# Kernel tuning notes

Hardware: AMD Instinct MI355X
Metric: run time of the kernel (lower is better)

The kernel has to match this reference:

```python
import jax, jax.numpy as jnp
import numpy as np

D = 768      # hidden_size
H = 12       # num_head
HD = D // H  # head_dim
LN_EPS = 1e-5


def setup_inputs() -> dict:
    key = jax.random.key(0)
    ks = jax.random.split(key, 9)
    N, S = 4, 2048
    s = 0.02
    return {
        "hidden_state": jax.random.normal(ks[0], (N, S, D), dtype=jnp.float32),
        "key_padding_mask": jax.random.randint(ks[1], (N, S), 0, 2, dtype=jnp.int64),
        "Wq": jax.random.normal(ks[2], (D, D), dtype=jnp.float32) * s,
        "Wk": jax.random.normal(ks[3], (D, D), dtype=jnp.float32) * s,
        "Wv": jax.random.normal(ks[4], (D, D), dtype=jnp.float32) * s,
        "Wo": jax.random.normal(ks[5], (D, D), dtype=jnp.float32) * s,
        "W1": jax.random.normal(ks[6], (4 * D, D), dtype=jnp.float32) * s,
        "W2": jax.random.normal(ks[7], (D, 4 * D), dtype=jnp.float32) * s,
        "ln_g": jnp.ones((D,), dtype=jnp.float32),
        "ln_b": jnp.zeros((D,), dtype=jnp.float32),
    }


def _layernorm(x, g, b):
    mu = jnp.mean(x, axis=-1, keepdims=True)
    var = jnp.mean(jnp.square(x - mu), axis=-1, keepdims=True)
    return (x - mu) * jax.lax.rsqrt(var + LN_EPS) * g + b


def reference(hidden_state, key_padding_mask, Wq, Wk, Wv, Wo, W1, W2, ln_g, ln_b):
    x = hidden_state
    N, S, _ = x.shape
    # Note: original module projects K and V from `query` (self-attention).
    def proj(W):
        return (x @ W.T).reshape(N, S, H, HD).transpose(0, 2, 1, 3)  # [N,H,S,HD]
    Q, K, V = proj(Wq), proj(Wk), proj(Wv)
    scores = jnp.einsum("bhqd,bhkd->bhqk", Q, K)  # [N,H,S,S]
    # int mask: 0 marks padding positions -> masked with -inf
    pad = (key_padding_mask == 0)[:, None, None, :]  # [N,1,1,S]
    scores = jnp.where(pad, -jnp.inf, scores)
    attn = jax.nn.softmax(scores / np.sqrt(HD), axis=-1)
    ctx = jnp.einsum("bhqk,bhkd->bhqd", attn, V)
    ctx = ctx.transpose(0, 2, 1, 3).reshape(N, S, D)
    mha = ctx @ Wo.T
    # residual + LayerNorm (same LN params used twice, as in the original)
    n1 = _layernorm(x + mha, ln_g, ln_b)
    # FFN with exact GELU (torch nn.GELU default)
    f = jax.nn.gelu(n1 @ W1.T, approximate=False) @ W2.T
    return _layernorm(n1 + f, ln_g, ln_b)
```

## Files before the change

kernel.cpp:

```cpp
#include <hip/hip_runtime.h>
#include <math.h>

typedef unsigned short u16;
typedef unsigned int u32;
typedef __bf16 bf16x8 __attribute__((ext_vector_type(8)));
typedef float f32x4 __attribute__((ext_vector_type(4)));

#define NB 4
#define SS 2048
#define DD 768
#define HH 12
#define HD 64
#define ROWS (NB*SS)

__device__ __forceinline__ u16 f2bf(float f) {
    union { float f; unsigned u; } v; v.f = f;
    unsigned r = v.u + 0x7fffu + ((v.u >> 16) & 1u);
    return (u16)(r >> 16);
}
__device__ __forceinline__ u32 fas(float f) { union { float f; u32 u; } v; v.f = f; return v.u; }

__device__ __forceinline__ void gl_lds16(const void* g, void* l) {
    __builtin_amdgcn_global_load_lds((__attribute__((address_space(1))) void*)(g),
                                     (__attribute__((address_space(3))) void*)(l),
                                     16, 0, 0);
}

__global__ __launch_bounds__(256) void prep_kernel(
        const float* __restrict__ X, const float* __restrict__ Wq,
        const float* __restrict__ Wk, const float* __restrict__ Wv,
        const float* __restrict__ Wo, const float* __restrict__ W1,
        const float* __restrict__ W2, const int* __restrict__ mask,
        u16* __restrict__ Xb, u16* __restrict__ Wqkvb, u16* __restrict__ Wob,
        u16* __restrict__ W1b, u16* __restrict__ W2b, float* __restrict__ mb) {
    const int blk = blockIdx.x, tid = threadIdx.x;
    const float* src; u16* dst; int idx;
    if (blk < 6144)       { src = X;  dst = Xb;               idx = blk * 1024 + tid * 4; }
    else if (blk < 6720)  { src = Wq; dst = Wqkvb;            idx = (blk - 6144) * 1024 + tid * 4; }
    else if (blk < 7296)  { src = Wk; dst = Wqkvb + DD * DD;  idx = (blk - 6720) * 1024 + tid * 4; }
    else if (blk < 7872)  { src = Wv; dst = Wqkvb + 2*DD*DD;  idx = (blk - 7296) * 1024 + tid * 4; }
    else if (blk < 8448)  { src = Wo; dst = Wob;              idx = (blk - 7872) * 1024 + tid * 4; }
    else if (blk < 10752) { src = W1; dst = W1b;              idx = (blk - 8448) * 1024 + tid * 4; }
    else if (blk < 13056) { src = W2; dst = W2b;              idx = (blk - 10752) * 1024 + tid * 4; }
    else {
        int i = (blk - 13056) * 1024 + tid * 4;
        float4 o;
        o.x = mask[i]     == 0 ? -1e30f : 0.0f;
        o.y = mask[i + 1] == 0 ? -1e30f : 0.0f;
        o.z = mask[i + 2] == 0 ? -1e30f : 0.0f;
        o.w = mask[i + 3] == 0 ? -1e30f : 0.0f;
        *(float4*)&mb[i] = o;
        return;
    }
    float4 v = *(const float4*)&src[idx];
    ushort4 o;
    o.x = f2bf(v.x); o.y = f2bf(v.y); o.z = f2bf(v.z); o.w = f2bf(v.w);
    *(ushort4*)&dst[idx] = o;
}

template <int EPI, int BN>
__global__ __launch_bounds__(256) void gemm_bt(const u16* __restrict__ A,
                                               const u16* __restrict__ B,
                                               int M, int N, int K,
                                               void* __restrict__ out,
                                               const void* __restrict__ aux,
                                               u16* __restrict__ Qb,
                                               u16* __restrict__ Kb,
                                               u16* __restrict__ Vb) {
    __shared__ __align__(16) u16 lA[128 * 64];
    __shared__ __align__(16) u16 lB[BN * 64];
    constexpr int MI = (BN == 128) ? 4 : 2;
    const int tid = threadIdx.x;
    const int lane = tid & 63, wave = tid >> 6;
    const int quad = lane >> 4, lc = lane & 15;
    const int m0 = blockIdx.y * 128, n0 = blockIdx.x * BN;
    const int wrow = (BN == 128) ? (wave >> 1) * 64 : wave * 32;
    const int wcol = (BN == 128) ? (wave & 1) * 64 : 0;
    const int swz = lc & 7;

    f32x4 acc[MI][4] = {};

    for (int kb = 0; kb < K; kb += 64) {
        __syncthreads();
#pragma unroll
        for (int p0 = 0; p0 < 1024; p0 += 256) {
            int p = p0 + tid, row = p >> 3, cl = (p & 7) ^ (row & 7);
            gl_lds16(A + (size_t)(m0 + row) * K + kb + cl * 8, &lA[(size_t)(p0 + wave * 64) * 8]);
        }
#pragma unroll
        for (int p0 = 0; p0 < BN * 8; p0 += 256) {
            int p = p0 + tid, row = p >> 3, cl = (p & 7) ^ (row & 7);
            gl_lds16(B + (size_t)(n0 + row) * K + kb + cl * 8, &lB[(size_t)(p0 + wave * 64) * 8]);
        }
        __syncthreads();
#pragma unroll
        for (int k2 = 0; k2 < 2; ++k2) {
            bf16x8 af[MI], bfr[4];
#pragma unroll
            for (int t = 0; t < MI; ++t)
                af[t] = *(const bf16x8*)&lA[(wrow + t * 16 + lc) * 64 + ((quad + k2 * 4) ^ swz) * 8];
#pragma unroll
            for (int t = 0; t < 4; ++t)
                bfr[t] = *(const bf16x8*)&lB[(wcol + t * 16 + lc) * 64 + ((quad + k2 * 4) ^ swz) * 8];
#pragma unroll
            for (int mi = 0; mi < MI; ++mi)
#pragma unroll
                for (int ni = 0; ni < 4; ++ni)
                    acc[mi][ni] = __builtin_amdgcn_mfma_f32_16x16x32_bf16(af[mi], bfr[ni],
                                                                         acc[mi][ni], 0, 0, 0);
        }
    }

#pragma unroll
    for (int mi = 0; mi < MI; ++mi) {
#pragma unroll
        for (int r = 0; r < 4; ++r) {
            int m = m0 + wrow + mi * 16 + quad * 4 + r;
#pragma unroll
            for (int ni = 0; ni < 4; ++ni) {
                int n = n0 + wcol + ni * 16 + lc;
                float v = acc[mi][ni][r];
                if constexpr (EPI == 0) {
                    int b = m >> 11, s = m & 2047;
                    int which = n / DD, rem = n - which * DD;
                    int h = rem >> 6, d = rem & 63;
                    u16* dst = which == 0 ? Qb : (which == 1 ? Kb : Vb);
                    dst[((((size_t)b * HH + h) * SS + s) << 6) + d] = f2bf(v);
                } else if constexpr (EPI == 1) {
                    float u = v * fmaf(v * v, 0.035677408f, 0.7978845608f);
                    float e = __builtin_amdgcn_exp2f(u * 2.885390082f);
                    float g = v - v * __builtin_amdgcn_rcpf(e + 1.0f);
                    ((u16*)out)[(size_t)m * N + n] = f2bf(g);
                } else if constexpr (EPI == 2) {
                    ((float*)out)[(size_t)m * N + n] =
                        v + ((const float*)aux)[(size_t)m * N + n];
                } else {
                    ((float*)out)[(size_t)m * N + n] =
                        v + (float)(((const __bf16*)aux)[(size_t)m * N + n]);
                }
            }
        }
    }
}

__global__ __launch_bounds__(256) void transpose_v(const u16* __restrict__ V,
                                                   u16* __restrict__ Vt) {
    __shared__ u16 t[32][33];
    int bh = blockIdx.z;
    int s0 = blockIdx.x * 32, d0 = blockIdx.y * 32;
    const u16* vb = V + (size_t)bh * SS * HD;
    u16* vtb = Vt + (size_t)bh * HD * SS;
    int tx = threadIdx.x & 31, ty = threadIdx.x >> 5;
#pragma unroll
    for (int i = 0; i < 32; i += 8) t[ty + i][tx] = vb[(size_t)(s0 + ty + i) * HD + d0 + tx];
    __syncthreads();
#pragma unroll
    for (int i = 0; i < 32; i += 8) vtb[(size_t)(d0 + ty + i) * SS + s0 + tx] = t[tx][ty + i];
}

__global__ __launch_bounds__(256) void attn_kernel(const u16* __restrict__ Q,
                                                   const u16* __restrict__ K,
                                                   const u16* __restrict__ Vt,
                                                   const float* __restrict__ maskbias,
                                                   u16* __restrict__ Ctx) {
    __shared__ __align__(16) u16 lK[2][64 * 64];
    __shared__ __align__(16) u16 lV[2][64 * 64];
    __shared__ __align__(16) u16 lP[4][32 * 72];
    const int tid = threadIdx.x, lane = tid & 63, wave = tid >> 6;
    const int quad = lane >> 4, lc = lane & 15;
    const int bh = blockIdx.x % (NB * HH);
    const int b = bh / HH, h = bh - b * HH;
    const int q0 = (blockIdx.x / (NB * HH)) * 128;
    const u16* Qg = Q + ((size_t)bh * SS + q0 + wave * 32) * HD;
    const u16* Kg = K + (size_t)bh * SS * HD;
    const u16* Vg = Vt + (size_t)bh * HD * SS;
    const float* mbg = maskbias + b * SS;
    const int sw = lc & 7;

    const int srow = tid >> 3, scl = (tid & 7) ^ (srow & 7);
    const int srow2 = (256 + tid) >> 3, scl2 = (tid & 7) ^ (srow2 & 7);

    bf16x8 qf[2][2];
#pragma unroll
    for (int mi = 0; mi < 2; ++mi)
#pragma unroll
        for (int k2 = 0; k2 < 2; ++k2)
            qf[mi][k2] = *(const bf16x8*)(Qg + (size_t)(mi * 16 + lc) * HD + k2 * 32 + quad * 8);

    bf16x8 onesf;
#pragma unroll
    for (int i = 0; i < 8; ++i) onesf[i] = (__bf16)1.0f;

    f32x4 oacc[2][4] = {};
    f32x4 lsum[2] = {};

    {
        gl_lds16(Kg + (size_t)srow * HD + scl * 8,        &lK[0][(size_t)(wave * 64) * 8]);
        gl_lds16(Vg + (size_t)srow * SS + scl * 8,        &lV[0][(size_t)(wave * 64) * 8]);
        gl_lds16(Kg + (size_t)srow2 * HD + scl2 * 8,      &lK[0][(size_t)(256 + wave * 64) * 8]);
        gl_lds16(Vg + (size_t)srow2 * SS + scl2 * 8,      &lV[0][(size_t)(256 + wave * 64) * 8]);
    }

    for (int j0 = 0; j0 < SS; j0 += 64) {
        const int cur = (j0 >> 6) & 1;
        __syncthreads();
        if (j0 + 64 < SS) {
            const int nxt = cur ^ 1;
            gl_lds16(Kg + (size_t)(j0 + 64 + srow) * HD + scl * 8,   &lK[nxt][(size_t)(wave * 64) * 8]);
            gl_lds16(Vg + (size_t)srow * SS + j0 + 64 + scl * 8,     &lV[nxt][(size_t)(wave * 64) * 8]);
            gl_lds16(Kg + (size_t)(j0 + 64 + srow2) * HD + scl2 * 8, &lK[nxt][(size_t)(256 + wave * 64) * 8]);
            gl_lds16(Vg + (size_t)srow2 * SS + j0 + 64 + scl2 * 8,   &lV[nxt][(size_t)(256 + wave * 64) * 8]);
        }

        f32x4 sacc[4][2] = {};
#pragma unroll
        for (int k2 = 0; k2 < 2; ++k2)
#pragma unroll
            for (int ni = 0; ni < 4; ++ni) {
                bf16x8 kf = *(const bf16x8*)&lK[cur][(ni * 16 + lc) * 64 + ((quad + k2 * 4) ^ sw) * 8];
                sacc[ni][0] = __builtin_amdgcn_mfma_f32_16x16x32_bf16(kf, qf[0][k2], sacc[ni][0], 0, 0, 0);
                sacc[ni][1] = __builtin_amdgcn_mfma_f32_16x16x32_bf16(kf, qf[1][k2], sacc[ni][1], 0, 0, 0);
            }

#pragma unroll
        for (int ni = 0; ni < 4; ++ni) {
            f32x4 mbv = *(const f32x4*)(mbg + j0 + ni * 16 + quad * 4);
#pragma unroll
            for (int mi = 0; mi < 2; ++mi) {
#pragma unroll
                for (int r = 0; r < 4; ++r)
                    sacc[ni][mi][r] = __builtin_amdgcn_exp2f(fmaf(sacc[ni][mi][r], 0.180336880f, mbv[r]));
                u32 w0 = __builtin_amdgcn_perm(fas(sacc[ni][mi][1]), fas(sacc[ni][mi][0]), 0x07060302);
                u32 w1 = __builtin_amdgcn_perm(fas(sacc[ni][mi][3]), fas(sacc[ni][mi][2]), 0x07060302);
                *(uint2*)&lP[wave][(mi * 16 + lc) * 72 + ni * 16 + quad * 4] = make_uint2(w0, w1);
            }
        }

#pragma unroll
        for (int k2 = 0; k2 < 2; ++k2) {
            bf16x8 pf0 = *(const bf16x8*)&lP[wave][(size_t)lc * 72 + k2 * 32 + quad * 8];
            bf16x8 pf1 = *(const bf16x8*)&lP[wave][(size_t)(16 + lc) * 72 + k2 * 32 + quad * 8];
            lsum[0] = __builtin_amdgcn_mfma_f32_16x16x32_bf16(pf0, onesf, lsum[0], 0, 0, 0);
            lsum[1] = __builtin_amdgcn_mfma_f32_16x16x32_bf16(pf1, onesf, lsum[1], 0, 0, 0);
#pragma unroll
            for (int ni = 0; ni < 4; ++ni) {
                bf16x8 vf = *(const bf16x8*)&lV[cur][(ni * 16 + lc) * 64 + ((quad + k2 * 4) ^ sw) * 8];
                oacc[0][ni] = __builtin_amdgcn_mfma_f32_16x16x32_bf16(pf0, vf, oacc[0][ni], 0, 0, 0);
                oacc[1][ni] = __builtin_amdgcn_mfma_f32_16x16x32_bf16(pf1, vf, oacc[1][ni], 0, 0, 0);
            }
        }
    }

#pragma unroll
    for (int mi = 0; mi < 2; ++mi)
#pragma unroll
        for (int r = 0; r < 4; ++r) {
            float inv = 1.0f / lsum[mi][r];
            int s = q0 + wave * 32 + mi * 16 + quad * 4 + r;
            size_t base = ((size_t)(b * SS + s)) * DD + h * HD;
#pragma unroll
            for (int ni = 0; ni < 4; ++ni)
                Ctx[base + ni * 16 + lc] = f2bf(oacc[mi][ni][r] * inv);
        }
}

__global__ __launch_bounds__(256) void ln_kernel(const float* __restrict__ in,
                                                 const float* __restrict__ g,
                                                 const float* __restrict__ bb,
                                                 u16* __restrict__ out_bf,
                                                 float* __restrict__ out_f) {
    const int row = blockIdx.x, tid = threadIdx.x;
    const float* x = in + (size_t)row * DD;
    float v0 = x[tid], v1 = x[tid + 256], v2 = x[tid + 512];
    float s = v0 + v1 + v2;
    float q = v0 * v0 + v1 * v1 + v2 * v2;
#pragma unroll
    for (int o = 1; o < 64; o <<= 1) {
        s += __shfl_xor(s, o);
        q += __shfl_xor(q, o);
    }
    __shared__ float rs[4], rq[4];
    int wave = tid >> 6;
    if ((tid & 63) == 0) { rs[wave] = s; rq[wave] = q; }
    __syncthreads();
    s = rs[0] + rs[1] + rs[2] + rs[3];
    q = rq[0] + rq[1] + rq[2] + rq[3];
    float mu = s * (1.0f / DD);
    float var = q * (1.0f / DD) - mu * mu;
    float rstd = rsqrtf(var + 1e-5f);
#pragma unroll
    for (int j = 0; j < 3; ++j) {
        int col = tid + j * 256;
        float v = (j == 0 ? v0 : (j == 1 ? v1 : v2));
        float y = (v - mu) * rstd * g[col] + bb[col];
        if (out_bf) out_bf[(size_t)row * DD + col] = f2bf(y);
        if (out_f) out_f[(size_t)row * DD + col] = y;
    }
}

extern "C" void kernel_launch(void* const* d_in, const int* in_sizes, int n_in,
                              void* d_out, int out_size, void* d_ws, size_t ws_size,
                              hipStream_t stream) {
    const float* X    = (const float*)d_in[0];
    const int*   mask = (const int*)d_in[1];
    const float* Wq   = (const float*)d_in[2];
    const float* Wk   = (const float*)d_in[3];
    const float* Wv   = (const float*)d_in[4];
    const float* Wo   = (const float*)d_in[5];
    const float* W1   = (const float*)d_in[6];
    const float* W2   = (const float*)d_in[7];
    const float* ln_g = (const float*)d_in[8];
    const float* ln_b = (const float*)d_in[9];
    float* out = (float*)d_out;

    char* ws = (char*)d_ws;
    size_t off = 0;
    auto alloc = [&](size_t bytes) {
        void* p = ws + off;
        off += (bytes + 255) & ~(size_t)255;
        return p;
    };
    u16*   Xbf   = (u16*)alloc((size_t)ROWS * DD * 2);
    u16*   Wqkvb = (u16*)alloc((size_t)3 * DD * DD * 2);
    u16*   Wob   = (u16*)alloc((size_t)DD * DD * 2);
    u16*   W1b   = (u16*)alloc((size_t)4 * DD * DD * 2);
    u16*   W2b   = (u16*)alloc((size_t)4 * DD * DD * 2);
    float* mbias = (float*)alloc((size_t)NB * SS * 4);
    u16*   Qb    = (u16*)alloc((size_t)ROWS * DD * 2);
    u16*   Kb    = (u16*)alloc((size_t)ROWS * DD * 2);
    u16*   Vb    = (u16*)alloc((size_t)ROWS * DD * 2);
    u16*   Vtb   = (u16*)alloc((size_t)ROWS * DD * 2);
    float* resid = (float*)alloc((size_t)ROWS * DD * 4);
    u16*   n1b   = (u16*)alloc((size_t)ROWS * DD * 2);
    u16*   Gb    = Qb;
    u16*   Ctxb  = Xbf;
    float* h2    = resid;

    prep_kernel<<<dim3(13064), dim3(256), 0, stream>>>(
        X, Wq, Wk, Wv, Wo, W1, W2, mask,
        Xbf, Wqkvb, Wob, W1b, W2b, mbias);

    gemm_bt<0, 128><<<dim3(3 * DD / 128, ROWS / 128), dim3(256), 0, stream>>>(
        Xbf, Wqkvb, ROWS, 3 * DD, DD, nullptr, nullptr, Qb, Kb, Vb);

    transpose_v<<<dim3(SS / 32, HD / 32, NB * HH), dim3(256), 0, stream>>>(Vb, Vtb);

    attn_kernel<<<dim3((SS / 128) * (NB * HH)), dim3(256), 0, stream>>>(
        Qb, Kb, Vtb, mbias, Ctxb);

    gemm_bt<2, 64><<<dim3(DD / 64, ROWS / 128), dim3(256), 0, stream>>>(
        Ctxb, Wob, ROWS, DD, DD, resid, X, nullptr, nullptr, nullptr);

    ln_kernel<<<dim3(ROWS), dim3(256), 0, stream>>>(resid, ln_g, ln_b, n1b, nullptr);

    gemm_bt<1, 128><<<dim3(4 * DD / 128, ROWS / 128), dim3(256), 0, stream>>>(
        n1b, W1b, ROWS, 4 * DD, DD, Gb, nullptr, nullptr, nullptr, nullptr);

    gemm_bt<3, 64><<<dim3(DD / 64, ROWS / 128), dim3(256), 0, stream>>>(
        Gb, W2b, ROWS, DD, 4 * DD, h2, n1b, nullptr, nullptr, nullptr);

    ln_kernel<<<dim3(ROWS), dim3(256), 0, stream>>>(h2, ln_g, ln_b, nullptr, out);
}
```

Before: 396.8 us.

## Remap GEMM tiles per XCD and drop attention K/V double buffering

GEMM launches now use a 1D grid, and the block index is remapped so that each of the 8 XCDs (round-robin by blockIdx) owns a contiguous group of 8 M-tiles. This is meant to improve L2 reuse of A rows within each XCD. The attention kernel replaces its double-buffered K/V LDS prefetch with a single buffer that is loaded and then synchronized each iteration. That halves K/V LDS use, which may raise occupancy, but it exposes load latency and adds a barrier per iteration.

After: 367.1 us. -7.5%, faster.

```diff
diff --git a/kernel.cpp b/kernel.cpp
--- a/kernel.cpp
+++ b/kernel.cpp
@@ -73,7 +73,9 @@
     const int tid = threadIdx.x;
     const int lane = tid & 63, wave = tid >> 6;
     const int quad = lane >> 4, lc = lane & 15;
-    const int m0 = blockIdx.y * 128, n0 = blockIdx.x * BN;
+    const int xcd = blockIdx.x & 7, loc = blockIdx.x >> 3;
+    const int mb = xcd * 8 + (loc & 7), nb = loc >> 3;
+    const int m0 = mb * 128, n0 = nb * BN;
     const int wrow = (BN == 128) ? (wave >> 1) * 64 : wave * 32;
     const int wcol = (BN == 128) ? (wave & 1) * 64 : 0;
     const int swz = lc & 7;
@@ -163,8 +165,8 @@
                                                    const u16* __restrict__ Vt,
                                                    const float* __restrict__ maskbias,
                                                    u16* __restrict__ Ctx) {
-    __shared__ __align__(16) u16 lK[2][64 * 64];
-    __shared__ __align__(16) u16 lV[2][64 * 64];
+    __shared__ __align__(16) u16 lK[64 * 64];
+    __shared__ __align__(16) u16 lV[64 * 64];
     __shared__ __align__(16) u16 lP[4][32 * 72];
     const int tid = threadIdx.x, lane = tid & 63, wave = tid >> 6;
     const int quad = lane >> 4, lc = lane & 15;
@@ -194,30 +196,20 @@
     f32x4 oacc[2][4] = {};
     f32x4 lsum[2] = {};
 
-    {
-        gl_lds16(Kg + (size_t)srow * HD + scl * 8,        &lK[0][(size_t)(wave * 64) * 8]);
-        gl_lds16(Vg + (size_t)srow * SS + scl * 8,        &lV[0][(size_t)(wave * 64) * 8]);
-        gl_lds16(Kg + (size_t)srow2 * HD + scl2 * 8,      &lK[0][(size_t)(256 + wave * 64) * 8]);
-        gl_lds16(Vg + (size_t)srow2 * SS + scl2 * 8,      &lV[0][(size_t)(256 + wave * 64) * 8]);
-    }
-
     for (int j0 = 0; j0 < SS; j0 += 64) {
-        const int cur = (j0 >> 6) & 1;
         __syncthreads();
-        if (j0 + 64 < SS) {
-            const int nxt = cur ^ 1;
-            gl_lds16(Kg + (size_t)(j0 + 64 + srow) * HD + scl * 8,   &lK[nxt][(size_t)(wave * 64) * 8]);
-            gl_lds16(Vg + (size_t)srow * SS + j0 + 64 + scl * 8,     &lV[nxt][(size_t)(wave * 64) * 8]);
-            gl_lds16(Kg + (size_t)(j0 + 64 + srow2) * HD + scl2 * 8, &lK[nxt][(size_t)(256 + wave * 64) * 8]);
-            gl_lds16(Vg + (size_t)srow2 * SS + j0 + 64 + scl2 * 8,   &lV[nxt][(size_t)(256 + wave * 64) * 8]);
-        }
+        gl_lds16(Kg + (size_t)(j0 + srow) * HD + scl * 8,   &lK[(size_t)(wave * 64) * 8]);
+        gl_lds16(Vg + (size_t)srow * SS + j0 + scl * 8,     &lV[(size_t)(wave * 64) * 8]);
+        gl_lds16(Kg + (size_t)(j0 + srow2) * HD + scl2 * 8, &lK[(size_t)(256 + wave * 64) * 8]);
+        gl_lds16(Vg + (size_t)srow2 * SS + j0 + scl2 * 8,   &lV[(size_t)(256 + wave * 64) * 8]);
+        __syncthreads();
 
         f32x4 sacc[4][2] = {};
 #pragma unroll
         for (int k2 = 0; k2 < 2; ++k2)
 #pragma unroll
             for (int ni = 0; ni < 4; ++ni) {
-                bf16x8 kf = *(const bf16x8*)&lK[cur][(ni * 16 + lc) * 64 + ((quad + k2 * 4) ^ sw) * 8];
+                bf16x8 kf = *(const bf16x8*)&lK[(ni * 16 + lc) * 64 + ((quad + k2 * 4) ^ sw) * 8];
                 sacc[ni][0] = __builtin_amdgcn_mfma_f32_16x16x32_bf16(kf, qf[0][k2], sacc[ni][0], 0, 0, 0);
                 sacc[ni][1] = __builtin_amdgcn_mfma_f32_16x16x32_bf16(kf, qf[1][k2], sacc[ni][1], 0, 0, 0);
             }
@@ -244,7 +236,7 @@
             lsum[1] = __builtin_amdgcn_mfma_f32_16x16x32_bf16(pf1, onesf, lsum[1], 0, 0, 0);
 #pragma unroll
             for (int ni = 0; ni < 4; ++ni) {
-                bf16x8 vf = *(const bf16x8*)&lV[cur][(ni * 16 + lc) * 64 + ((quad + k2 * 4) ^ sw) * 8];
+                bf16x8 vf = *(const bf16x8*)&lV[(ni * 16 + lc) * 64 + ((quad + k2 * 4) ^ sw) * 8];
                 oacc[0][ni] = __builtin_amdgcn_mfma_f32_16x16x32_bf16(pf0, vf, oacc[0][ni], 0, 0, 0);
                 oacc[1][ni] = __builtin_amdgcn_mfma_f32_16x16x32_bf16(pf1, vf, oacc[1][ni], 0, 0, 0);
             }
@@ -340,7 +332,7 @@
         X, Wq, Wk, Wv, Wo, W1, W2, mask,
         Xbf, Wqkvb, Wob, W1b, W2b, mbias);
 
-    gemm_bt<0, 128><<<dim3(3 * DD / 128, ROWS / 128), dim3(256), 0, stream>>>(
+    gemm_bt<0, 128><<<dim3((3 * DD / 128) * (ROWS / 128)), dim3(256), 0, stream>>>(
         Xbf, Wqkvb, ROWS, 3 * DD, DD, nullptr, nullptr, Qb, Kb, Vb);
 
     transpose_v<<<dim3(SS / 32, HD / 32, NB * HH), dim3(256), 0, stream>>>(Vb, Vtb);
@@ -348,15 +340,15 @@
     attn_kernel<<<dim3((SS / 128) * (NB * HH)), dim3(256), 0, stream>>>(
         Qb, Kb, Vtb, mbias, Ctxb);
 
-    gemm_bt<2, 64><<<dim3(DD / 64, ROWS / 128), dim3(256), 0, stream>>>(
+    gemm_bt<2, 64><<<dim3((DD / 64) * (ROWS / 128)), dim3(256), 0, stream>>>(
         Ctxb, Wob, ROWS, DD, DD, resid, X, nullptr, nullptr, nullptr);
 
     ln_kernel<<<dim3(ROWS), dim3(256), 0, stream>>>(resid, ln_g, ln_b, n1b, nullptr);
 
-    gemm_bt<1, 128><<<dim3(4 * DD / 128, ROWS / 128), dim3(256), 0, stream>>>(
+    gemm_bt<1, 128><<<dim3((4 * DD / 128) * (ROWS / 128)), dim3(256), 0, stream>>>(
         n1b, W1b, ROWS, 4 * DD, DD, Gb, nullptr, nullptr, nullptr, nullptr);
 
-    gemm_bt<3, 64><<<dim3(DD / 64, ROWS / 128), dim3(256), 0, stream>>>(
+    gemm_bt<3, 64><<<dim3((DD / 64) * (ROWS / 128)), dim3(256), 0, stream>>>(
         Gb, W2b, ROWS, DD, 4 * DD, h2, n1b, nullptr, nullptr, nullptr);
 
     ln_kernel<<<dim3(ROWS), dim3(256), 0, stream>>>(h2, ln_g, ln_b, nullptr, out);
```
